# Optimization experiments

Hardware: AMD Instinct MI355X
Metric: run time of the kernel (lower is better)

The kernel has to match this reference:

```python
import jax, jax.numpy as jnp
import numpy as np
import math

B, L, C = 8, 1024, 256
H, CH = 8, 32  # num_heads, c_hidden; H*CH == C


def setup_inputs() -> dict:
    key = jax.random.key(0)
    ks = jax.random.split(key, 8)
    s = 0.02
    return {
        "q_x": jax.random.normal(ks[0], (B, L, C), jnp.float32),
        "bias_mask": jnp.zeros((B, 1, 1, L), jnp.float32),
        "bias_pair": jax.random.normal(ks[1], (B, H, L, L), jnp.float32),
        "Wq": jax.random.normal(ks[2], (C, H * CH), jnp.float32) * s,
        "Wk": jax.random.normal(ks[3], (C, H * CH), jnp.float32) * s,
        "Wv": jax.random.normal(ks[4], (C, H * CH), jnp.float32) * s,
        "Wg": jax.random.normal(ks[5], (C, H * CH), jnp.float32) * s,
        "bg": jnp.ones((H * CH,), jnp.float32),  # gating bias init = 1 in AlphaFold
        "Wo": jax.random.normal(ks[6], (H * CH, C), jnp.float32) * s,
        "bo": jnp.zeros((C,), jnp.float32),
    }


def reference(q_x, bias_mask, bias_pair, Wq, Wk, Wv, Wg, bg, Wo, bo):
    # QKV projections (self-attention: kv_x = q_x), split heads -> [B, H, L, CH]
    def proj(W):
        return (q_x @ W).reshape(B, L, H, CH).transpose(0, 2, 1, 3)

    q = proj(Wq) / math.sqrt(CH)
    k = proj(Wk)
    v = proj(Wv)

    # scores + multi-bias add, stable softmax over keys
    a = jnp.einsum("bhqc,bhkc->bhqk", q, k) + bias_mask + bias_pair
    a = jax.nn.softmax(a, axis=-1)

    # weighted values -> [B, L, H, CH]
    o = jnp.einsum("bhqk,bhkc->bhqc", a, v).transpose(0, 2, 1, 3)

    # sigmoid gating from query data
    g = jax.nn.sigmoid(q_x @ Wg + bg).reshape(B, L, H, CH)
    o = o * g

    # merge heads and output projection
    o = o.reshape(B, L, H * CH)
    return o @ Wo + bo
```

## Files before the change

kernel.cpp:

```cpp
#include <hip/hip_runtime.h>
#include <hip/hip_bf16.h>
#include <hip/hip_fp16.h>
#include <math.h>

#define BB 8
#define LL 1024
#define CC 256
#define HH 8
#define CHD 32

typedef __attribute__((ext_vector_type(8))) _Float16 half8;
typedef __attribute__((ext_vector_type(4))) float f32x4;
typedef __attribute__((ext_vector_type(4))) unsigned int u32x4;

#define MFMA16 __builtin_amdgcn_mfma_f32_16x16x32_f16
#define LO_SCALE 2048.f
#define LO_INV   4.8828125e-4f

__device__ __forceinline__ float u2f(unsigned short u) {
    return __uint_as_float(((unsigned)u) << 16);
}
__device__ __forceinline__ float ldv(const void* p, size_t i, bool f32) {
    return f32 ? ((const float*)p)[i] : u2f(((const unsigned short*)p)[i]);
}
__device__ __forceinline__ float4 ldv4(const void* p, size_t i, bool f32) {
    if (f32) return *(const float4*)((const float*)p + i);
    ushort4 u = *(const ushort4*)((const unsigned short*)p + i);
    return make_float4(u2f(u.x), u2f(u.y), u2f(u.z), u2f(u.w));
}
__device__ __forceinline__ bool probe_f32(const void* bg) {
    return *(const unsigned*)bg == 0x3F800000u;
}
__device__ __forceinline__ unsigned pack_h2(float a, float b) {
    __half2 h = __floats2half2_rn(a, b);
    return *(unsigned*)&h;
}
__device__ __forceinline__ void store_h4(__half* p, float a, float b, float c, float d) {
    uint2 u = make_uint2(pack_h2(a, b), pack_h2(c, d));
    *(uint2*)p = u;
}
__device__ __forceinline__ void cvt_store_hilo(__half* ph, __half* pl, float4 v) {
    __half2 a = __floats2half2_rn(v.x, v.y), b2 = __floats2half2_rn(v.z, v.w);
    *(uint2*)ph = make_uint2(*(unsigned*)&a, *(unsigned*)&b2);
    float rx = (v.x - __low2float(a))  * LO_SCALE;
    float ry = (v.y - __high2float(a)) * LO_SCALE;
    float rz = (v.z - __low2float(b2)) * LO_SCALE;
    float rw = (v.w - __high2float(b2)) * LO_SCALE;
    __half2 c = __floats2half2_rn(rx, ry), d = __floats2half2_rn(rz, rw);
    *(uint2*)pl = make_uint2(*(unsigned*)&c, *(unsigned*)&d);
}

__global__ __launch_bounds__(256) void prep_w_kernel(
    const void* __restrict__ Wq, const void* __restrict__ Wk,
    const void* __restrict__ Wv, const void* __restrict__ Wg,
    const void* __restrict__ Wo, const void* __restrict__ bg,
    __half* __restrict__ wt_hi, __half* __restrict__ wt_lo)
{
    const bool f32 = probe_f32(bg);
    const int blk = blockIdx.x;
    const int mi = blk >> 6, tile = blk & 63;
    const void* W = (mi == 0) ? Wq : (mi == 1) ? Wk : (mi == 2) ? Wv
                  : (mi == 3) ? Wg : Wo;
    const int tr = tile >> 3, tc = tile & 7;
    __shared__ float ts[32][33];
    const int t = threadIdx.x;
    for (int e = t; e < 1024; e += 256) {
        const int r = e >> 5, c = e & 31;
        ts[r][c] = ldv(W, (size_t)(32 * tr + r) * 256 + 32 * tc + c, f32);
    }
    __syncthreads();
    for (int e = t; e < 1024; e += 256) {
        const int r = e >> 5, c = e & 31;
        const float v = ts[c][r];
        const __half h = __float2half(v);
        const __half l = __float2half((v - __half2float(h)) * LO_SCALE);
        const size_t o = (size_t)mi * 65536 + (size_t)(32 * tc + r) * 256 + 32 * tr + c;
        wt_hi[o] = h;
        wt_lo[o] = l;
    }
}

__global__ __launch_bounds__(256) void proj_mfma_kernel(
    const void* __restrict__ qx,
    const __half* __restrict__ wt_hi, const __half* __restrict__ wt_lo,
    const void* __restrict__ bg,
    __half* __restrict__ q_ws, __half* __restrict__ k_ws,
    __half* __restrict__ vt_ws, __half* __restrict__ g_ws)
{
    const bool f32 = probe_f32(bg);
    __shared__ __align__(16) __half xhi[32][264];
    __shared__ __align__(16) __half xlo[32][264];
    const int t   = threadIdx.x;
    const int m0  = blockIdx.x * 32;
    const int mat = blockIdx.y;

    for (int e = t; e < 2048; e += 256) {
        const int r = e >> 6, c4 = e & 63;
        float4 v = ldv4(qx, (size_t)(m0 + r) * CC + (size_t)c4 * 4, f32);
        cvt_store_hilo(&xhi[r][c4 * 4], &xlo[r][c4 * 4], v);
    }
    __syncthreads();

    const int ln = t & 63, wv = t >> 6;
    const int lq = ln & 15, g = ln >> 4;
    const int nb = 64 * wv;
    const __half* bh_base = wt_hi + (size_t)mat * 65536
                          + (size_t)(nb + lq) * 256 + 8 * g;
    const __half* bl_base = wt_lo + (size_t)mat * 65536
                          + (size_t)(nb + lq) * 256 + 8 * g;

    f32x4 accm[2][4], accc[2][4];
#pragma unroll
    for (int ms = 0; ms < 2; ++ms)
#pragma unroll
        for (int j = 0; j < 4; ++j) {
            accm[ms][j] = (f32x4){0.f, 0.f, 0.f, 0.f};
            accc[ms][j] = (f32x4){0.f, 0.f, 0.f, 0.f};
        }

    const bool vmat = (mat == 2);
#pragma unroll
    for (int kc = 0; kc < 8; ++kc) {
        half8 bh[4], bl[4];
#pragma unroll
        for (int j = 0; j < 4; ++j) {
            bh[j] = *(const half8*)(bh_base + j * 4096 + kc * 32);
            bl[j] = *(const half8*)(bl_base + j * 4096 + kc * 32);
        }
#pragma unroll
        for (int ms = 0; ms < 2; ++ms) {
            const half8 ah = *(const half8*)&xhi[ms * 16 + lq][kc * 32 + 8 * g];
            const half8 al = *(const half8*)&xlo[ms * 16 + lq][kc * 32 + 8 * g];
#pragma unroll
            for (int j = 0; j < 4; ++j) {
                if (!vmat) {
                    accm[ms][j] = MFMA16(bh[j], ah, accm[ms][j], 0, 0, 0);
                    accc[ms][j] = MFMA16(bl[j], ah, accc[ms][j], 0, 0, 0);
                    accc[ms][j] = MFMA16(bh[j], al, accc[ms][j], 0, 0, 0);
                } else {
                    accm[ms][j] = MFMA16(ah, bh[j], accm[ms][j], 0, 0, 0);
                    accc[ms][j] = MFMA16(al, bh[j], accc[ms][j], 0, 0, 0);
                    accc[ms][j] = MFMA16(ah, bl[j], accc[ms][j], 0, 0, 0);
                }
            }
        }
    }

    const int b  = m0 >> 10;
    const int l0 = m0 & 1023;

    if (mat == 3) {
#pragma unroll
        for (int ms = 0; ms < 2; ++ms) {
            const int m = m0 + ms * 16 + lq;
#pragma unroll
            for (int j = 0; j < 4; ++j) {
                const int n0 = nb + 16 * j + 4 * g;
                float4 bgv = ldv4(bg, n0, f32);
                float z0 = accm[ms][j].x + accc[ms][j].x * LO_INV + bgv.x;
                float z1 = accm[ms][j].y + accc[ms][j].y * LO_INV + bgv.y;
                float z2 = accm[ms][j].z + accc[ms][j].z * LO_INV + bgv.z;
                float z3 = accm[ms][j].w + accc[ms][j].w * LO_INV + bgv.w;
                store_h4(g_ws + (size_t)m * 256 + n0,
                         1.f / (1.f + __expf(-z0)), 1.f / (1.f + __expf(-z1)),
                         1.f / (1.f + __expf(-z2)), 1.f / (1.f + __expf(-z3)));
            }
        }
    } else if (vmat) {
#pragma unroll
        for (int ms = 0; ms < 2; ++ms)
#pragma unroll
            for (int j = 0; j < 4; ++j) {
                const int n = nb + 16 * j + lq, h = n >> 5, ch = n & 31;
                __half* dst = vt_ws + ((size_t)(b * HH + h) * CHD + ch) * LL
                            + l0 + ms * 16 + 4 * g;
                store_h4(dst,
                         accm[ms][j].x + accc[ms][j].x * LO_INV,
                         accm[ms][j].y + accc[ms][j].y * LO_INV,
                         accm[ms][j].z + accc[ms][j].z * LO_INV,
                         accm[ms][j].w + accc[ms][j].w * LO_INV);
            }
    } else {
        const float scale = (mat == 0) ? 0.17677669529663687f : 1.f;
        __half* dst0 = (mat == 0) ? q_ws : k_ws;
#pragma unroll
        for (int ms = 0; ms < 2; ++ms) {
            const int l = l0 + ms * 16 + lq;
#pragma unroll
            for (int j = 0; j < 4; ++j) {
                const int n0 = nb + 16 * j + 4 * g, h = n0 >> 5, ch = n0 & 31;
                __half* dst = dst0 + ((size_t)(b * HH + h) * LL + l) * CHD + ch;
                store_h4(dst,
                         (accm[ms][j].x + accc[ms][j].x * LO_INV) * scale,
                         (accm[ms][j].y + accc[ms][j].y * LO_INV) * scale,
                         (accm[ms][j].z + accc[ms][j].z * LO_INV) * scale,
                         (accm[ms][j].w + accc[ms][j].w * LO_INV) * scale);
            }
        }
    }
}

__global__ __launch_bounds__(256) void attn_mfma_kernel(
    const __half* __restrict__ q_ws, const __half* __restrict__ k_ws,
    const __half* __restrict__ vt_ws, const __half* __restrict__ g_ws,
    const void* __restrict__ mask, const void* __restrict__ bias,
    const void* __restrict__ bg,
    float* __restrict__ og_out)
{
    const bool f32 = probe_f32(bg);
    const int t  = threadIdx.x;
    const int wv = t >> 6;
    const int ln = t & 63;
    const int lq = ln & 15;
    const int g  = ln >> 4;
    const int bh = blockIdx.y;
    const int b  = bh >> 3, h = bh & 7;
    const int q0 = blockIdx.x * 64 + wv * 16;
    const int qi = q0 + lq;

    const half8 qfrag = *(const half8*)(q_ws + ((size_t)bh * LL + qi) * CHD + 8 * g);

    f32x4 o0 = {0.f, 0.f, 0.f, 0.f};
    f32x4 o1 = {0.f, 0.f, 0.f, 0.f};
    float m_run = -1e30f, l_run = 0.f;

    const size_t bias_base = ((size_t)bh * LL + qi) * LL;
    const size_t mask_base = (size_t)b * LL;
    const f32x4 zz = {0.f, 0.f, 0.f, 0.f};

    float4 b4c[4];
#pragma unroll
    for (int s = 0; s < 4; ++s)
        b4c[s] = ldv4(bias, bias_base + 16 * s + 4 * g, f32);

    for (int k0 = 0; k0 < LL; k0 += 64) {
        f32x4 sc[4];
#pragma unroll
        for (int s = 0; s < 4; ++s) {
            half8 kf = *(const half8*)(k_ws +
                ((size_t)bh * LL + k0 + 16 * s + lq) * CHD + 8 * g);
            sc[s] = MFMA16(kf, qfrag, zz, 0, 0, 0);
        }
        const int kn = (k0 + 64 < LL) ? (k0 + 64) : k0;
        float4 b4n[4];
#pragma unroll
        for (int s = 0; s < 4; ++s)
            b4n[s] = ldv4(bias, bias_base + kn + 16 * s + 4 * g, f32);
#pragma unroll
        for (int s = 0; s < 4; ++s) {
            float4 m4 = ldv4(mask, mask_base + k0 + 16 * s + 4 * g, f32);
            sc[s].x += b4c[s].x + m4.x;
            sc[s].y += b4c[s].y + m4.y;
            sc[s].z += b4c[s].z + m4.z;
            sc[s].w += b4c[s].w + m4.w;
        }
        float mt = fmaxf(fmaxf(sc[0].x, sc[0].y), fmaxf(sc[0].z, sc[0].w));
#pragma unroll
        for (int s = 1; s < 4; ++s)
            mt = fmaxf(mt, fmaxf(fmaxf(sc[s].x, sc[s].y), fmaxf(sc[s].z, sc[s].w)));
        mt = fmaxf(mt, __shfl_xor(mt, 16));
        mt = fmaxf(mt, __shfl_xor(mt, 32));
        const float mn = fmaxf(m_run, mt);
        const float alpha = __expf(m_run - mn);
        m_run = mn;
        float ls = 0.f;
#pragma unroll
        for (int s = 0; s < 4; ++s) {
            sc[s].x = __expf(sc[s].x - mn); ls += sc[s].x;
            sc[s].y = __expf(sc[s].y - mn); ls += sc[s].y;
            sc[s].z = __expf(sc[s].z - mn); ls += sc[s].z;
            sc[s].w = __expf(sc[s].w - mn); ls += sc[s].w;
        }
        ls += __shfl_xor(ls, 16);
        ls += __shfl_xor(ls, 32);
        l_run = l_run * alpha + ls;
        o0 = o0 * alpha;
        o1 = o1 * alpha;

        unsigned ph[4][2];
#pragma unroll
        for (int s = 0; s < 4; ++s) {
            ph[s][0] = pack_h2(sc[s].x, sc[s].y);
            ph[s][1] = pack_h2(sc[s].z, sc[s].w);
        }
#pragma unroll
        for (int tt = 0; tt < 2; ++tt) {
            unsigned bfr[4];
#pragma unroll
            for (int w = 0; w < 4; ++w) {
                const int src = lq + 16 * (2 * (g & 1) + (w >> 1));
                unsigned lo = (unsigned)__shfl((int)ph[2 * tt + 0][w & 1], src);
                unsigned hi = (unsigned)__shfl((int)ph[2 * tt + 1][w & 1], src);
                bfr[w] = (g >= 2) ? hi : lo;
            }
            u32x4 bv = {bfr[0], bfr[1], bfr[2], bfr[3]};
            half8 pB = __builtin_bit_cast(half8, bv);
            half8 vf0 = *(const half8*)(vt_ws +
                ((size_t)bh * CHD + lq) * LL + k0 + 32 * tt + 8 * g);
            o0 = MFMA16(vf0, pB, o0, 0, 0, 0);
            half8 vf1 = *(const half8*)(vt_ws +
                ((size_t)bh * CHD + 16 + lq) * LL + k0 + 32 * tt + 8 * g);
            o1 = MFMA16(vf1, pB, o1, 0, 0, 0);
        }
#pragma unroll
        for (int s = 0; s < 4; ++s) b4c[s] = b4n[s];
    }

    const float inv = 1.f / l_run;
    const size_t row = (size_t)b * LL + qi;
    const __half* gp = g_ws + row * CC + h * CHD + 4 * g;
    float* op = og_out + row * CC + h * CHD + 4 * g;
    float4 r0, r1;
    r0.x = o0.x * inv * __half2float(gp[0]);
    r0.y = o0.y * inv * __half2float(gp[1]);
    r0.z = o0.z * inv * __half2float(gp[2]);
    r0.w = o0.w * inv * __half2float(gp[3]);
    r1.x = o1.x * inv * __half2float(gp[16]);
    r1.y = o1.y * inv * __half2float(gp[17]);
    r1.z = o1.z * inv * __half2float(gp[18]);
    r1.w = o1.w * inv * __half2float(gp[19]);
    *(float4*)op = r0;
    *(float4*)(op + 16) = r1;
}

__global__ __launch_bounds__(256) void out_mfma_kernel(
    float* __restrict__ io,
    const __half* __restrict__ wt_hi, const __half* __restrict__ wt_lo,
    const void* __restrict__ bo, const void* __restrict__ bg)
{
    const bool f32 = probe_f32(bg);
    __shared__ __align__(16) __half xhi[16][264];
    __shared__ __align__(16) __half xlo[16][264];
    const int t  = threadIdx.x;
    const int m0 = blockIdx.x * 16;

    for (int e = t; e < 1024; e += 256) {
        const int r = e >> 6, c4 = e & 63;
        float4 v = *(const float4*)(io + (size_t)(m0 + r) * CC + (size_t)c4 * 4);
        cvt_store_hilo(&xhi[r][c4 * 4], &xlo[r][c4 * 4], v);
    }
    __syncthreads();

    const int ln = t & 63, wv = t >> 6;
    const int lq = ln & 15, g = ln >> 4;
    const __half* bh_base = wt_hi + (size_t)4 * 65536 + (size_t)lq * 256 + 8 * g;
    const __half* bl_base = wt_lo + (size_t)4 * 65536 + (size_t)lq * 256 + 8 * g;

    f32x4 accm[4], accc[4];
#pragma unroll
    for (int j = 0; j < 4; ++j) {
        accm[j] = (f32x4){0.f, 0.f, 0.f, 0.f};
        accc[j] = (f32x4){0.f, 0.f, 0.f, 0.f};
    }

    for (int kc = 0; kc < 8; ++kc) {
        const half8 ah = *(const half8*)&xhi[lq][kc * 32 + 8 * g];
        const half8 al = *(const half8*)&xlo[lq][kc * 32 + 8 * g];
#pragma unroll
        for (int j = 0; j < 4; ++j) {
            const int nt = wv * 4 + j;
            const half8 bh = *(const half8*)(bh_base + nt * 4096 + kc * 32);
            const half8 bl = *(const half8*)(bl_base + nt * 4096 + kc * 32);
            accm[j] = MFMA16(bh, ah, accm[j], 0, 0, 0);
            accc[j] = MFMA16(bl, ah, accc[j], 0, 0, 0);
            accc[j] = MFMA16(bh, al, accc[j], 0, 0, 0);
        }
    }

    const int m = m0 + lq;
#pragma unroll
    for (int j = 0; j < 4; ++j) {
        const int n0 = (wv * 4 + j) * 16 + 4 * g;
        float4 bov = ldv4(bo, n0, f32);
        float4 r;
        r.x = accm[j].x + accc[j].x * LO_INV + bov.x;
        r.y = accm[j].y + accc[j].y * LO_INV + bov.y;
        r.z = accm[j].z + accc[j].z * LO_INV + bov.z;
        r.w = accm[j].w + accc[j].w * LO_INV + bov.w;
        *(float4*)(io + (size_t)m * 256 + n0) = r;
    }
}

extern "C" void kernel_launch(void* const* d_in, const int* in_sizes, int n_in,
                              void* d_out, int out_size, void* d_ws, size_t ws_size,
                              hipStream_t stream) {
    const void* qx   = d_in[0];
    const void* mask = d_in[1];
    const void* bias = d_in[2];
    const void* Wq   = d_in[3];
    const void* Wk   = d_in[4];
    const void* Wv   = d_in[5];
    const void* Wg   = d_in[6];
    const void* bg   = d_in[7];
    const void* Wo   = d_in[8];
    const void* bo   = d_in[9];
    float* out = (float*)d_out;

    char* ws = (char*)d_ws;
    const size_t TEN = (size_t)BB * LL * CC * sizeof(__half);
    __half* q_ws  = (__half*)(ws + 0 * TEN);
    __half* k_ws  = (__half*)(ws + 1 * TEN);
    __half* vt_ws = (__half*)(ws + 2 * TEN);
    __half* g_ws  = (__half*)(ws + 3 * TEN);
    __half* wt_hi = (__half*)(ws + 4 * TEN);
    __half* wt_lo = (__half*)(ws + 4 * TEN + (size_t)2 * 1024 * 1024);

    prep_w_kernel<<<dim3(320), 256, 0, stream>>>(Wq, Wk, Wv, Wg, Wo, bg,
                                                 wt_hi, wt_lo);
    proj_mfma_kernel<<<dim3(256, 4), 256, 0, stream>>>(qx, wt_hi, wt_lo, bg,
                                                       q_ws, k_ws, vt_ws, g_ws);
    attn_mfma_kernel<<<dim3(16, 64), 256, 0, stream>>>(q_ws, k_ws, vt_ws, g_ws,
                                                       mask, bias, bg, out);
    out_mfma_kernel<<<dim3(512), 256, 0, stream>>>(out, wt_hi, wt_lo, bo, bg);
}
```

Baseline: 484.0 us.

## Stage mask in LDS, prefetch K/V fragments, double M-tile in output projection

```diff
diff --git a/kernel.cpp b/kernel.cpp
--- a/kernel.cpp
+++ b/kernel.cpp
@@ -208,6 +208,7 @@
     float* __restrict__ og_out)
 {
     const bool f32 = probe_f32(bg);
+    __shared__ __align__(16) float mask_s[LL];
     const int t  = threadIdx.x;
     const int wv = t >> 6;
     const int ln = t & 63;
@@ -218,6 +219,11 @@
     const int q0 = blockIdx.x * 64 + wv * 16;
     const int qi = q0 + lq;
 
+    {
+        float4 mv = ldv4(mask, (size_t)b * LL + t * 4, f32);
+        *(float4*)&mask_s[t * 4] = mv;
+    }
+
     const half8 qfrag = *(const half8*)(q_ws + ((size_t)bh * LL + qi) * CHD + 8 * g);
 
     f32x4 o0 = {0.f, 0.f, 0.f, 0.f};
@@ -225,7 +231,6 @@
     float m_run = -1e30f, l_run = 0.f;
 
     const size_t bias_base = ((size_t)bh * LL + qi) * LL;
-    const size_t mask_base = (size_t)b * LL;
     const f32x4 zz = {0.f, 0.f, 0.f, 0.f};
 
     float4 b4c[4];
@@ -233,22 +238,36 @@
     for (int s = 0; s < 4; ++s)
         b4c[s] = ldv4(bias, bias_base + 16 * s + 4 * g, f32);
 
+    __syncthreads();
+
     for (int k0 = 0; k0 < LL; k0 += 64) {
-        f32x4 sc[4];
-#pragma unroll
-        for (int s = 0; s < 4; ++s) {
-            half8 kf = *(const half8*)(k_ws +
+        half8 kf[4];
+#pragma unroll
+        for (int s = 0; s < 4; ++s)
+            kf[s] = *(const half8*)(k_ws +
                 ((size_t)bh * LL + k0 + 16 * s + lq) * CHD + 8 * g);
-            sc[s] = MFMA16(kf, qfrag, zz, 0, 0, 0);
+        half8 vfr[4];
+#pragma unroll
+        for (int tt = 0; tt < 2; ++tt) {
+            vfr[2 * tt]     = *(const half8*)(vt_ws +
+                ((size_t)bh * CHD + lq) * LL + k0 + 32 * tt + 8 * g);
+            vfr[2 * tt + 1] = *(const half8*)(vt_ws +
+                ((size_t)bh * CHD + 16 + lq) * LL + k0 + 32 * tt + 8 * g);
         }
         const int kn = (k0 + 64 < LL) ? (k0 + 64) : k0;
         float4 b4n[4];
 #pragma unroll
         for (int s = 0; s < 4; ++s)
             b4n[s] = ldv4(bias, bias_base + kn + 16 * s + 4 * g, f32);
+
+        f32x4 sc[4];
+#pragma unroll
+        for (int s = 0; s < 4; ++s)
+            sc[s] = MFMA16(kf[s], qfrag, zz, 0, 0, 0);
+
 #pragma unroll
         for (int s = 0; s < 4; ++s) {
-            float4 m4 = ldv4(mask, mask_base + k0 + 16 * s + 4 * g, f32);
+            const float4 m4 = *(const float4*)&mask_s[k0 + 16 * s + 4 * g];
             sc[s].x += b4c[s].x + m4.x;
             sc[s].y += b4c[s].y + m4.y;
             sc[s].z += b4c[s].z + m4.z;
@@ -295,12 +314,8 @@
             }
             u32x4 bv = {bfr[0], bfr[1], bfr[2], bfr[3]};
             half8 pB = __builtin_bit_cast(half8, bv);
-            half8 vf0 = *(const half8*)(vt_ws +
-                ((size_t)bh * CHD + lq) * LL + k0 + 32 * tt + 8 * g);
-            o0 = MFMA16(vf0, pB, o0, 0, 0, 0);
-            half8 vf1 = *(const half8*)(vt_ws +
-                ((size_t)bh * CHD + 16 + lq) * LL + k0 + 32 * tt + 8 * g);
-            o1 = MFMA16(vf1, pB, o1, 0, 0, 0);
+            o0 = MFMA16(vfr[2 * tt],     pB, o0, 0, 0, 0);
+            o1 = MFMA16(vfr[2 * tt + 1], pB, o1, 0, 0, 0);
         }
 #pragma unroll
         for (int s = 0; s < 4; ++s) b4c[s] = b4n[s];
@@ -329,12 +344,12 @@
     const void* __restrict__ bo, const void* __restrict__ bg)
 {
     const bool f32 = probe_f32(bg);
-    __shared__ __align__(16) __half xhi[16][264];
-    __shared__ __align__(16) __half xlo[16][264];
+    __shared__ __align__(16) __half xhi[32][264];
+    __shared__ __align__(16) __half xlo[32][264];
     const int t  = threadIdx.x;
-    const int m0 = blockIdx.x * 16;
-
-    for (int e = t; e < 1024; e += 256) {
+    const int m0 = blockIdx.x * 32;
+
+    for (int e = t; e < 2048; e += 256) {
         const int r = e >> 6, c4 = e & 63;
         float4 v = *(const float4*)(io + (size_t)(m0 + r) * CC + (size_t)c4 * 4);
         cvt_store_hilo(&xhi[r][c4 * 4], &xlo[r][c4 * 4], v);
@@ -343,41 +358,54 @@
 
     const int ln = t & 63, wv = t >> 6;
     const int lq = ln & 15, g = ln >> 4;
-    const __half* bh_base = wt_hi + (size_t)4 * 65536 + (size_t)lq * 256 + 8 * g;
-    const __half* bl_base = wt_lo + (size_t)4 * 65536 + (size_t)lq * 256 + 8 * g;
-
-    f32x4 accm[4], accc[4];
-#pragma unroll
-    for (int j = 0; j < 4; ++j) {
-        accm[j] = (f32x4){0.f, 0.f, 0.f, 0.f};
-        accc[j] = (f32x4){0.f, 0.f, 0.f, 0.f};
-    }
-
+    const int nb = 64 * wv;
+    const __half* bh_base = wt_hi + (size_t)4 * 65536 + (size_t)(nb + lq) * 256 + 8 * g;
+    const __half* bl_base = wt_lo + (size_t)4 * 65536 + (size_t)(nb + lq) * 256 + 8 * g;
+
+    f32x4 accm[2][4], accc[2][4];
+#pragma unroll
+    for (int ms = 0; ms < 2; ++ms)
+#pragma unroll
+        for (int j = 0; j < 4; ++j) {
+            accm[ms][j] = (f32x4){0.f, 0.f, 0.f, 0.f};
+            accc[ms][j] = (f32x4){0.f, 0.f, 0.f, 0.f};
+        }
+
+#pragma unroll
     for (int kc = 0; kc < 8; ++kc) {
-        const half8 ah = *(const half8*)&xhi[lq][kc * 32 + 8 * g];
-        const half8 al = *(const half8*)&xlo[lq][kc * 32 + 8 * g];
+        half8 bh[4], bl[4];
 #pragma unroll
         for (int j = 0; j < 4; ++j) {
-            const int nt = wv * 4 + j;
-            const half8 bh = *(const half8*)(bh_base + nt * 4096 + kc * 32);
-            const half8 bl = *(const half8*)(bl_base + nt * 4096 + kc * 32);
-            accm[j] = MFMA16(bh, ah, accm[j], 0, 0, 0);
-            accc[j] = MFMA16(bl, ah, accc[j], 0, 0, 0);
-            accc[j] = MFMA16(bh, al, accc[j], 0, 0, 0);
-        }
-    }
-
-    const int m = m0 + lq;
-#pragma unroll
-    for (int j = 0; j < 4; ++j) {
-        const int n0 = (wv * 4 + j) * 16 + 4 * g;
-        float4 bov = ldv4(bo, n0, f32);
-        float4 r;
-        r.x = accm[j].x + accc[j].x * LO_INV + bov.x;
-        r.y = accm[j].y + accc[j].y * LO_INV + bov.y;
-        r.z = accm[j].z + accc[j].z * LO_INV + bov.z;
-        r.w = accm[j].w + accc[j].w * LO_INV + bov.w;
-        *(float4*)(io + (size_t)m * 256 + n0) = r;
+            bh[j] = *(const half8*)(bh_base + j * 4096 + kc * 32);
+            bl[j] = *(const half8*)(bl_base + j * 4096 + kc * 32);
+        }
+#pragma unroll
+        for (int ms = 0; ms < 2; ++ms) {
+            const half8 ah = *(const half8*)&xhi[ms * 16 + lq][kc * 32 + 8 * g];
+            const half8 al = *(const half8*)&xlo[ms * 16 + lq][kc * 32 + 8 * g];
+#pragma unroll
+            for (int j = 0; j < 4; ++j) {
+                accm[ms][j] = MFMA16(bh[j], ah, accm[ms][j], 0, 0, 0);
+                accc[ms][j] = MFMA16(bl[j], ah, accc[ms][j], 0, 0, 0);
+                accc[ms][j] = MFMA16(bh[j], al, accc[ms][j], 0, 0, 0);
+            }
+        }
+    }
+
+#pragma unroll
+    for (int ms = 0; ms < 2; ++ms) {
+        const int m = m0 + ms * 16 + lq;
+#pragma unroll
+        for (int j = 0; j < 4; ++j) {
+            const int n0 = nb + 16 * j + 4 * g;
+            float4 bov = ldv4(bo, n0, f32);
+            float4 r;
+            r.x = accm[ms][j].x + accc[ms][j].x * LO_INV + bov.x;
+            r.y = accm[ms][j].y + accc[ms][j].y * LO_INV + bov.y;
+            r.z = accm[ms][j].z + accc[ms][j].z * LO_INV + bov.z;
+            r.w = accm[ms][j].w + accc[ms][j].w * LO_INV + bov.w;
+            *(float4*)(io + (size_t)m * 256 + n0) = r;
+        }
     }
 }
 
@@ -411,5 +439,5 @@
                                                        q_ws, k_ws, vt_ws, g_ws);
     attn_mfma_kernel<<<dim3(16, 64), 256, 0, stream>>>(q_ws, k_ws, vt_ws, g_ws,
                                                        mask, bias, bg, out);
-    out_mfma_kernel<<<dim3(512), 256, 0, stream>>>(out, wt_hi, wt_lo, bo, bg);
-}
+    out_mfma_kernel<<<dim3(256), 256, 0, stream>>>(out, wt_hi, wt_lo, bo, bg);
+}
```

Result: faster. 472.4 us (-2.4%).
